# Performance work log

Measured on AMD Instinct MI355X. Metric: run time of the kernel, lower is better.

Reference implementation:

```python
import jax, jax.numpy as jnp
from jax import lax
import numpy as np

B, DIM, H, W = 8, 192, 128, 128
HEADS = 4


def setup_inputs() -> dict:
    key = jax.random.key(0)
    k1, k2, k3, k4 = jax.random.split(key, 4)
    x = jax.random.normal(k1, (B, DIM, H, W), dtype=jnp.float32)
    w_qkv = jax.random.normal(k2, (2 * DIM, DIM), dtype=jnp.float32) * 0.05
    w_dw = jax.random.normal(k3, (2 * DIM, 1, 3, 3), dtype=jnp.float32) * 0.1
    w_proj = jax.random.normal(k4, (DIM, DIM), dtype=jnp.float32) * 0.05
    temperature = jnp.ones((HEADS, 1, 1), dtype=jnp.float32)
    return {"x": x, "w_qkv": w_qkv, "w_dw": w_dw, "w_proj": w_proj, "temperature": temperature}


def reference(x, w_qkv, w_dw, w_proj, temperature):
    b, c, h, w = x.shape
    heads = temperature.shape[0]
    head_c = c // heads
    # 1x1 conv: dim -> 2*dim
    qkv = jnp.einsum('oc,bchw->bohw', w_qkv, x)
    # 3x3 depthwise conv over 2*dim channels
    qkv = lax.conv_general_dilated(
        qkv, w_dw, window_strides=(1, 1), padding='SAME',
        feature_group_count=2 * c,
        dimension_numbers=('NCHW', 'OIHW', 'NCHW'))
    q, v = jnp.split(qkv, 2, axis=1)
    # [b, heads, head_c, h*w]
    q = q.reshape(b, heads, head_c, h * w)
    v = v.reshape(b, heads, head_c, h * w)
    # L2-normalize q over spatial dim; k = q
    q = q / jnp.linalg.norm(q, axis=-1, keepdims=True)
    # channel-wise attention: [b, heads, head_c, head_c]
    attn = jnp.einsum('bhcn,bhdn->bhcd', q, q) * temperature[None]
    attn = jax.nn.softmax(attn, axis=-1)
    out = jnp.einsum('bhcd,bhdn->bhcn', attn, v)
    out = out.reshape(b, c, h, w)
    # 1x1 projection
    return jnp.einsum('oc,bchw->bohw', w_proj, out)
```

## Files before the change

kernel.cpp:

```cpp
#include <hip/hip_runtime.h>

#define BB 8
#define CC 192
#define C2 384
#define HH 128
#define WW 128
#define NN 16384
#define NHEADS 4
#define HC 48
#define LTK 196
#define LTK2 98

typedef float f32x2 __attribute__((ext_vector_type(2)));
typedef float f32x4 __attribute__((ext_vector_type(4)));
typedef float f32x16 __attribute__((ext_vector_type(16)));
typedef short s16x4 __attribute__((ext_vector_type(4)));
typedef short s16x8 __attribute__((ext_vector_type(8)));
typedef unsigned short u16;
typedef u16 u16x4 __attribute__((ext_vector_type(4)));
typedef u16 u16x8 __attribute__((ext_vector_type(8)));
typedef unsigned int u32;

__device__ __forceinline__ float bfu2f(u32 u16v) {
  return __uint_as_float(u16v << 16);
}
__device__ __forceinline__ u16 f2bfu(float f) {
  u32 u = __float_as_uint(f);
  return (u16)((u + 0x7fffu + ((u >> 16) & 1u)) >> 16);
}
__device__ __forceinline__ s16x8 ldpair(const u16* p) {
  s16x4 lo = *reinterpret_cast<const s16x4*>(p);
  s16x4 hi = *reinterpret_cast<const s16x4*>(p + 16);
  return __builtin_shufflevector(lo, hi, 0, 1, 2, 3, 4, 5, 6, 7);
}
__device__ __forceinline__ s16x8 ldb64pair(const u32* p) {
  s16x4 lo = *reinterpret_cast<const s16x4*>(p);
  s16x4 hi = *reinterpret_cast<const s16x4*>(p + 2);
  return __builtin_shufflevector(lo, hi, 0, 1, 2, 3, 4, 5, 6, 7);
}

__global__ __launch_bounds__(256) void k0_wcvt(const float* __restrict__ w,
                                               u16* __restrict__ wbf) {
  const int i = (blockIdx.x * 256 + threadIdx.x) * 4;
  f32x4 v = *reinterpret_cast<const f32x4*>(&w[i]);
  u16x4 o;
  o[0] = f2bfu(v[0]); o[1] = f2bfu(v[1]); o[2] = f2bfu(v[2]); o[3] = f2bfu(v[3]);
  *reinterpret_cast<u16x4*>(&wbf[i]) = o;
}

__global__ __launch_bounds__(512, 4) void k1_qkv(
    const float* __restrict__ x, const u16* __restrict__ wbf,
    u16* __restrict__ qkv) {
  const int bx = blockIdx.x;
  const int n0 = (((bx & 7) << 4) + (bx >> 3)) << 7;
  const int b  = blockIdx.y;
  __shared__ u16 Xs[128 * LTK];
  u32* Xsw = reinterpret_cast<u32*>(Xs);
  const int t = threadIdx.x, lane = t & 63;
  const int wid = t >> 6, wo = wid >> 1, wn = wid & 1;
  const int l31 = lane & 31, g2 = lane >> 5;

  {
    const int nq = t & 31, cr = t >> 5;
    const int kpb = cr >> 1;
    const int jh = cr & 1;
    const int prA = 2 * nq + jh;
    const int prB = 64 + 2 * nq + jh;
    const float* xb = x + (size_t)b * CC * NN + n0 + 4 * nq;
    #pragma unroll 6
    for (int i = 0; i < 12; ++i) {
      f32x4 v = *reinterpret_cast<const f32x4*>(xb + (size_t)(cr + 16 * i) * NN);
      u32 A  = (u32)f2bfu(v[0]) | ((u32)f2bfu(v[1]) << 16);
      u32 Bp = (u32)f2bfu(v[2]) | ((u32)f2bfu(v[3]) << 16);
      u32 oA = __shfl_xor(A, 32);
      u32 oB = __shfl_xor(Bp, 32);
      u32 va, vb;
      if (jh) {
        va = (oB & 0xffffu) | (Bp << 16);
        vb = (oB >> 16) | (Bp & 0xffff0000u);
      } else {
        va = (A & 0xffffu) | (oA << 16);
        vb = (A >> 16) | (oA & 0xffff0000u);
      }
      const int col = kpb + 8 * i;
      Xsw[prA * LTK2 + col] = va;
      Xsw[prB * LTK2 + col] = vb;
    }
  }
  __syncthreads();

  const int nb2 = wn * 32;
  const u32* browE = &Xsw[(nb2 + l31) * LTK2 + 4 * g2];
  const u32* browO = &Xsw[(64 + nb2 + l31) * LTK2 + 4 * g2];

  for (int ot = 0; ot < 3; ++ot) {
    const int o0 = ot * 128;
    const u16* wr = wbf + (size_t)(o0 + wo * 32 + l31) * CC + 8 * g2;

    s16x8 afA[6], afB[6];
    #pragma unroll
    for (int s = 0; s < 6; ++s) {
      afA[s] = *reinterpret_cast<const s16x8*>(wr + s * 32);
      afB[s] = *reinterpret_cast<const s16x8*>(wr + s * 32 + 16);
    }

    f32x16 accE, accO;
    #pragma unroll
    for (int e = 0; e < 16; ++e) { accE[e] = 0.f; accO[e] = 0.f; }

    #pragma unroll
    for (int s = 0; s < 6; ++s) {
      s16x8 bfE0 = ldb64pair(browE + 16 * s);
      s16x8 bfE1 = ldb64pair(browE + 16 * s + 8);
      s16x8 bfO0 = ldb64pair(browO + 16 * s);
      s16x8 bfO1 = ldb64pair(browO + 16 * s + 8);
      accE = __builtin_amdgcn_mfma_f32_32x32x16_bf16(afA[s], bfE0, accE, 0, 0, 0);
      accO = __builtin_amdgcn_mfma_f32_32x32x16_bf16(afA[s], bfO0, accO, 0, 0, 0);
      accE = __builtin_amdgcn_mfma_f32_32x32x16_bf16(afB[s], bfE1, accE, 0, 0, 0);
      accO = __builtin_amdgcn_mfma_f32_32x32x16_bf16(afB[s], bfO1, accO, 0, 0, 0);
    }
    #pragma unroll
    for (int r = 0; r < 16; ++r) {
      const int row = (r & 3) + 8 * (r >> 2) + 4 * g2;
      const u32 pk = (u32)f2bfu(accE[r]) | ((u32)f2bfu(accO[r]) << 16);
      *reinterpret_cast<u32*>(
          &qkv[((size_t)b * C2 + o0 + wo * 32 + row) * NN + n0 + wn * 64 + 2 * l31]) = pk;
    }
  }
}

__global__ __launch_bounds__(256) void k2_dw(
    const u16* __restrict__ qkv, const float* __restrict__ wdw,
    u16* __restrict__ out) {
  const int gid = blockIdx.x;
  const int rb = gid & 7;
  const int p = gid >> 3;
  const int b = p / 192, cv = p % 192;
  const int ch = CC + cv;
  const int plane = b * C2 + ch;
  const int t = threadIdx.x;
  const int row = rb * 16 + (t >> 4);
  const int x0 = (t & 15) * 8;
  const u16* pp = qkv + (size_t)plane * NN;
  const float* wv = wdw + ch * 9;
  float o[8];
  #pragma unroll
  for (int j = 0; j < 8; ++j) o[j] = 0.f;
  #pragma unroll
  for (int dy = 0; dy < 3; ++dy) {
    const int yy = row + dy - 1;
    if ((unsigned)yy < (unsigned)HH) {
      const u16* rp = pp + yy * WW;
      u16x8 m = *reinterpret_cast<const u16x8*>(&rp[x0]);
      float px[10];
      px[0] = (x0 > 0) ? bfu2f(rp[x0 - 1]) : 0.f;
      px[9] = (x0 < 120) ? bfu2f(rp[x0 + 8]) : 0.f;
      #pragma unroll
      for (int j = 0; j < 8; ++j) px[j + 1] = bfu2f(m[j]);
      const float w0 = wv[dy * 3 + 0], w1 = wv[dy * 3 + 1], w2 = wv[dy * 3 + 2];
      #pragma unroll
      for (int j = 0; j < 8; ++j)
        o[j] += w0 * px[j] + w1 * px[j + 1] + w2 * px[j + 2];
    }
  }
  u16x8 ov;
  #pragma unroll
  for (int j = 0; j < 8; ++j) ov[j] = f2bfu(o[j]);
  *reinterpret_cast<u16x8*>(&out[(size_t)plane * NN + row * WW + x0]) = ov;
}

__global__ __launch_bounds__(256, 2) void k23_convgram(
    const u16* __restrict__ qkv, const float* __restrict__ wdw,
    float* __restrict__ gpart) {
  const int raw = blockIdx.x;
  const int rp = ((raw & 7) << 3) + (raw >> 3);
  const int h = blockIdx.y, b = blockIdx.z;
  __shared__ u16 inq[48 * 520];
  __shared__ float wsm[432];
  __shared__ u16 qd[48 * 264];
  const int t = threadIdx.x, lane = t & 63, wv = t >> 6;
  const int l15 = lane & 15, g = lane >> 4;
  const u16* qb = qkv + ((size_t)b * C2 + h * HC) * NN;

  for (int idx = t; idx < 432; idx += 256) wsm[idx] = wdw[h * 432 + idx];
  #pragma unroll
  for (int it = 0; it < 12; ++it) {
    const int idx = t + 256 * it;
    const int ch = idx >> 6, rem = idx & 63;
    const int iy = rem >> 4, grp = rem & 15;
    const int gy = 2 * rp - 1 + iy;
    u16x8 v;
    #pragma unroll
    for (int e = 0; e < 8; ++e) v[e] = 0;
    if ((unsigned)gy < (unsigned)HH)
      v = *reinterpret_cast<const u16x8*>(qb + (size_t)ch * NN + gy * WW + grp * 8);
    *reinterpret_cast<u16x8*>(&inq[ch * 520 + iy * 128 + grp * 8]) = v;
  }
  __syncthreads();

  #pragma unroll
  for (int it = 0; it < 6; ++it) {
    const int idx = t + 256 * it;
    const int ch = idx >> 5, grp = idx & 31;
    const int p0 = grp * 8;
    const int orow = p0 >> 7, x0 = p0 & 127;
    float o[8];
    #pragma unroll
    for (int j = 0; j < 8; ++j) o[j] = 0.f;
    #pragma unroll
    for (int dy = 0; dy < 3; ++dy) {
      const u16* rp_ = &inq[ch * 520 + (orow + dy) * 128];
      u16x8 m = *reinterpret_cast<const u16x8*>(&rp_[x0]);
      float px[10];
      px[0] = (x0 > 0) ? bfu2f(rp_[x0 - 1]) : 0.f;
      px[9] = (x0 < 120) ? bfu2f(rp_[x0 + 8]) : 0.f;
      #pragma unroll
      for (int j = 0; j < 8; ++j) px[j + 1] = bfu2f(m[j]);
      const float w0 = wsm[ch * 9 + dy * 3 + 0];
      const float w1 = wsm[ch * 9 + dy * 3 + 1];
      const float w2 = wsm[ch * 9 + dy * 3 + 2];
      #pragma unroll
      for (int j = 0; j < 8; ++j)
        o[j] += w0 * px[j] + w1 * px[j + 1] + w2 * px[j + 2];
    }
    u16x8 ov;
    #pragma unroll
    for (int j = 0; j < 8; ++j) ov[j] = f2bfu(o[j]);
    *reinterpret_cast<u16x8*>(&qd[ch * 264 + p0]) = ov;
  }
  __syncthreads();

  f32x4 acc[3][3];
  #pragma unroll
  for (int i = 0; i < 3; ++i)
    #pragma unroll
    for (int j = 0; j < 3; ++j)
      #pragma unroll
      for (int e = 0; e < 4; ++e) acc[i][j][e] = 0.f;

  #pragma unroll
  for (int s = 0; s < 2; ++s) {
    const int n = wv * 64 + s * 32;
    s16x8 cf[3];
    #pragma unroll
    for (int i = 0; i < 3; ++i)
      cf[i] = ldpair(&qd[(i * 16 + l15) * 264 + n + 4 * g]);
    #pragma unroll
    for (int i = 0; i < 3; ++i)
      #pragma unroll
      for (int j = 0; j < 3; ++j)
        acc[i][j] = __builtin_amdgcn_mfma_f32_16x16x32_bf16(cf[i], cf[j], acc[i][j], 0, 0, 0);
  }

  float* red = reinterpret_cast<float*>(inq);
  #pragma unroll
  for (int i = 0; i < 3; ++i)
    #pragma unroll
    for (int j = 0; j < 3; ++j)
      #pragma unroll
      for (int r = 0; r < 4; ++r)
        red[wv * 2304 + (i * 16 + 4 * g + r) * 48 + j * 16 + l15] = acc[i][j][r];
  __syncthreads();
  float* gp = gpart + (size_t)b * 3145728 + h * 147456 + rp * 2304;
  for (int idx = t; idx < 2304; idx += 256)
    gp[idx] = red[idx] + red[2304 + idx] + red[4608 + idx] + red[6912 + idx];
}

__global__ __launch_bounds__(256) void k4_soft(
    const float* __restrict__ gpart, const float* __restrict__ temp,
    float* __restrict__ attn) {
  const int bh = blockIdx.x;
  const int b = bh >> 2, h = bh & 3;
  const int t = threadIdx.x;
  __shared__ float G[2304];
  __shared__ float rn[48];
  const float* gp = gpart + (size_t)b * 3145728 + h * 147456;
  for (int idx = t; idx < 2304; idx += 256) {
    float s = 0.f;
    #pragma unroll 8
    for (int c = 0; c < 64; ++c) s += gp[c * 2304 + idx];
    G[idx] = s;
  }
  __syncthreads();
  if (t < 48) rn[t] = rsqrtf(G[t * 48 + t]);
  __syncthreads();
  if (t < 48) {
    const float tm = temp[h];
    float v[48];
    float mx = -1e30f;
    #pragma unroll
    for (int j = 0; j < 48; ++j) {
      v[j] = G[t * 48 + j] * rn[t] * rn[j] * tm;
      mx = fmaxf(mx, v[j]);
    }
    float s = 0.f;
    #pragma unroll
    for (int j = 0; j < 48; ++j) { v[j] = expf(v[j] - mx); s += v[j]; }
    const float inv = 1.f / s;
    #pragma unroll
    for (int j = 0; j < 48; ++j)
      attn[(size_t)bh * 2304 + t * 48 + j] = v[j] * inv;
  }
}

__global__ __launch_bounds__(192) void k5_M(
    const float* __restrict__ wproj, const float* __restrict__ attn,
    u16* __restrict__ Mbf) {
  const int o = blockIdx.x;
  const int b = blockIdx.y;
  const int d = threadIdx.x;
  const int h = d / HC, dl = d % HC;
  const float* wrow = wproj + o * CC + h * HC;
  const float* at = attn + ((size_t)(b * NHEADS + h)) * 2304;
  float s = 0.f;
  #pragma unroll
  for (int c = 0; c < HC; ++c) s = fmaf(wrow[c], at[c * HC + dl], s);
  Mbf[((size_t)b * CC + o) * CC + d] = f2bfu(s);
}

__global__ __launch_bounds__(256, 4) void k6_out(
    const u16* __restrict__ Mbf, const u16* __restrict__ qkvd,
    float* __restrict__ out) {
  const int bx = blockIdx.x;
  const int n0 = (((bx & 7) << 4) + (bx >> 3)) << 7;
  const int b  = blockIdx.y;
  __shared__ u16 Vs[128 * LTK];
  u32* Vsw = reinterpret_cast<u32*>(Vs);
  const int t = threadIdx.x, lane = t & 63;
  const int wid = t >> 6, wo = wid >> 1, wn = wid & 1;
  const int l31 = lane & 31, g2 = lane >> 5;

  {
    const int nq = t & 31, cr = t >> 5;
    const int kpb = cr >> 1;
    const int jh = cr & 1;
    const int prA = 2 * nq + jh;
    const int prB = 64 + 2 * nq + jh;
    const u16* vbp = qkvd + ((size_t)b * C2 + CC) * NN + n0 + 4 * nq;
    #pragma unroll 6
    for (int i = 0; i < 24; ++i) {
      u16x4 m = *reinterpret_cast<const u16x4*>(vbp + (size_t)(cr + 8 * i) * NN);
      u32 A  = (u32)m[0] | ((u32)m[1] << 16);
      u32 Bp = (u32)m[2] | ((u32)m[3] << 16);
      u32 oA = __shfl_xor(A, 32);
      u32 oB = __shfl_xor(Bp, 32);
      u32 va, vb;
      if (jh) {
        va = (oB & 0xffffu) | (Bp << 16);
        vb = (oB >> 16) | (Bp & 0xffff0000u);
      } else {
        va = (A & 0xffffu) | (oA << 16);
        vb = (A >> 16) | (oA & 0xffff0000u);
      }
      const int col = kpb + 4 * i;
      Vsw[prA * LTK2 + col] = va;
      Vsw[prB * LTK2 + col] = vb;
    }
  }
  __syncthreads();

  const int nb2 = wn * 32;
  const u32* browE = &Vsw[(nb2 + l31) * LTK2 + 4 * g2];
  const u32* browO = &Vsw[(64 + nb2 + l31) * LTK2 + 4 * g2];
  const u16* Ab = Mbf + (size_t)b * CC * CC;

  for (int ot = 0; ot < 3; ++ot) {
    const int o0 = ot * 64;
    const u16* ar = Ab + (size_t)(o0 + wo * 32 + l31) * CC + 8 * g2;

    s16x8 afA[6], afB[6];
    #pragma unroll
    for (int s = 0; s < 6; ++s) {
      afA[s] = *reinterpret_cast<const s16x8*>(ar + s * 32);
      afB[s] = *reinterpret_cast<const s16x8*>(ar + s * 32 + 16);
    }

    f32x16 accE, accO;
    #pragma unroll
    for (int e = 0; e < 16; ++e) { accE[e] = 0.f; accO[e] = 0.f; }

    #pragma unroll
    for (int s = 0; s < 6; ++s) {
      s16x8 bfE0 = ldb64pair(browE + 16 * s);
      s16x8 bfE1 = ldb64pair(browE + 16 * s + 8);
      s16x8 bfO0 = ldb64pair(browO + 16 * s);
      s16x8 bfO1 = ldb64pair(browO + 16 * s + 8);
      accE = __builtin_amdgcn_mfma_f32_32x32x16_bf16(afA[s], bfE0, accE, 0, 0, 0);
      accO = __builtin_amdgcn_mfma_f32_32x32x16_bf16(afA[s], bfO0, accO, 0, 0, 0);
      accE = __builtin_amdgcn_mfma_f32_32x32x16_bf16(afB[s], bfE1, accE, 0, 0, 0);
      accO = __builtin_amdgcn_mfma_f32_32x32x16_bf16(afB[s], bfO1, accO, 0, 0, 0);
    }
    #pragma unroll
    for (int r = 0; r < 16; ++r) {
      const int row = (r & 3) + 8 * (r >> 2) + 4 * g2;
      f32x2 st;
      st[0] = accE[r];
      st[1] = accO[r];
      f32x2* op = reinterpret_cast<f32x2*>(
          &out[((size_t)b * CC + o0 + wo * 32 + row) * NN + n0 + wn * 64 + 2 * l31]);
      __builtin_nontemporal_store(st, op);
    }
  }
}

extern "C" void kernel_launch(void* const* d_in, const int* in_sizes, int n_in,
                              void* d_out, int out_size, void* d_ws, size_t ws_size,
                              hipStream_t stream) {
  const float* x      = (const float*)d_in[0];
  const float* w_qkv  = (const float*)d_in[1];
  const float* w_dw   = (const float*)d_in[2];
  const float* w_proj = (const float*)d_in[3];
  const float* temp   = (const float*)d_in[4];
  float* out = (float*)d_out;

  const size_t OFF_QKV   = 0;
  const size_t OFF_QKVD  = 100663296ULL;
  const size_t OFF_ATTN  = 206045184ULL;
  const size_t OFF_M     = 206340096ULL;
  const size_t OFF_WBF   = 206929920ULL;
  const size_t NEEDED    = 207077376ULL;
  if (ws_size < NEEDED) return;

  char* ws = (char*)d_ws;
  u16* qkv   = (u16*)(ws + OFF_QKV);
  u16* qkvd  = (u16*)(ws + OFF_QKVD);
  float* gpart = (float*)(ws + OFF_QKVD);
  float* attn  = (float*)(ws + OFF_ATTN);
  u16* Mbf   = (u16*)(ws + OFF_M);
  u16* wbf   = (u16*)(ws + OFF_WBF);

  k0_wcvt<<<dim3(72), 256, 0, stream>>>(w_qkv, wbf);
  k1_qkv <<<dim3(128, 8), 512, 0, stream>>>(x, wbf, qkv);
  k2_dw  <<<dim3(BB * 192 * 8), 256, 0, stream>>>(qkv, w_dw, qkvd);
  k23_convgram<<<dim3(64, NHEADS, BB), 256, 0, stream>>>(qkv, w_dw, gpart);
  k4_soft<<<dim3(BB * NHEADS), 256, 0, stream>>>(gpart, temp, attn);
  k5_M   <<<dim3(CC, BB), 192, 0, stream>>>(w_proj, attn, Mbf);
  k6_out <<<dim3(128, 8), 256, 0, stream>>>(Mbf, qkvd, out);
}
```

Before: 223.6 us.

## Store qkv and dw-conv output in row-blocked layout for contiguous per-row access

Changes the intermediate qkv and depthwise-conv buffers from channel-plane NCHW to a [b][row][channel][128] blocked layout. k1 writes each 128-pixel row tile for all channels into one contiguous block, and k2 is reorganised to process one image row across all v channels. k23 and k6 read the new layout so their strided loads become contiguous chunks. The gpart region moves to its own offset with a smaller per-batch stride. This is meant to improve DRAM locality of writes and reads across the pipeline, at the cost of k2 doing more work per block and k23 halo loads touching separate blocks.

```diff
diff --git a/kernel.cpp b/kernel.cpp
--- a/kernel.cpp
+++ b/kernel.cpp
@@ -50,9 +50,10 @@
 
 __global__ __launch_bounds__(512, 4) void k1_qkv(
     const float* __restrict__ x, const u16* __restrict__ wbf,
-    u16* __restrict__ qkv) {
+    u16* __restrict__ qblk) {
   const int bx = blockIdx.x;
-  const int n0 = (((bx & 7) << 4) + (bx >> 3)) << 7;
+  const int p0 = ((bx & 7) << 4) + (bx >> 3);
+  const int n0 = p0 << 7;
   const int b  = blockIdx.y;
   __shared__ u16 Xs[128 * LTK];
   u32* Xsw = reinterpret_cast<u32*>(Xs);
@@ -92,6 +93,7 @@
   const int nb2 = wn * 32;
   const u32* browE = &Xsw[(nb2 + l31) * LTK2 + 4 * g2];
   const u32* browO = &Xsw[(64 + nb2 + l31) * LTK2 + 4 * g2];
+  u16* dstbase = qblk + ((size_t)(b * 128 + p0) * C2) * 128;
 
   for (int ot = 0; ot < 3; ++ot) {
     const int o0 = ot * 128;
@@ -124,53 +126,54 @@
       const int row = (r & 3) + 8 * (r >> 2) + 4 * g2;
       const u32 pk = (u32)f2bfu(accE[r]) | ((u32)f2bfu(accO[r]) << 16);
       *reinterpret_cast<u32*>(
-          &qkv[((size_t)b * C2 + o0 + wo * 32 + row) * NN + n0 + wn * 64 + 2 * l31]) = pk;
+          &dstbase[(o0 + wo * 32 + row) * 128 + wn * 64 + 2 * l31]) = pk;
     }
   }
 }
 
 __global__ __launch_bounds__(256) void k2_dw(
-    const u16* __restrict__ qkv, const float* __restrict__ wdw,
-    u16* __restrict__ out) {
-  const int gid = blockIdx.x;
-  const int rb = gid & 7;
-  const int p = gid >> 3;
-  const int b = p / 192, cv = p % 192;
-  const int ch = CC + cv;
-  const int plane = b * C2 + ch;
+    const u16* __restrict__ qblk, const float* __restrict__ wdw,
+    u16* __restrict__ vblk) {
+  const int y = blockIdx.x;
+  const int b = blockIdx.y;
   const int t = threadIdx.x;
-  const int row = rb * 16 + (t >> 4);
-  const int x0 = (t & 15) * 8;
-  const u16* pp = qkv + (size_t)plane * NN;
-  const float* wv = wdw + ch * 9;
-  float o[8];
-  #pragma unroll
-  for (int j = 0; j < 8; ++j) o[j] = 0.f;
-  #pragma unroll
-  for (int dy = 0; dy < 3; ++dy) {
-    const int yy = row + dy - 1;
-    if ((unsigned)yy < (unsigned)HH) {
-      const u16* rp = pp + yy * WW;
-      u16x8 m = *reinterpret_cast<const u16x8*>(&rp[x0]);
-      float px[10];
-      px[0] = (x0 > 0) ? bfu2f(rp[x0 - 1]) : 0.f;
-      px[9] = (x0 < 120) ? bfu2f(rp[x0 + 8]) : 0.f;
-      #pragma unroll
-      for (int j = 0; j < 8; ++j) px[j + 1] = bfu2f(m[j]);
-      const float w0 = wv[dy * 3 + 0], w1 = wv[dy * 3 + 1], w2 = wv[dy * 3 + 2];
-      #pragma unroll
-      for (int j = 0; j < 8; ++j)
-        o[j] += w0 * px[j] + w1 * px[j + 1] + w2 * px[j + 2];
-    }
-  }
-  u16x8 ov;
-  #pragma unroll
-  for (int j = 0; j < 8; ++j) ov[j] = f2bfu(o[j]);
-  *reinterpret_cast<u16x8*>(&out[(size_t)plane * NN + row * WW + x0]) = ov;
+  #pragma unroll
+  for (int it = 0; it < 12; ++it) {
+    const int idx = t + 256 * it;
+    const int ch = idx >> 4;
+    const int grp = idx & 15;
+    const int x0 = grp * 8;
+    const float* wv = wdw + (CC + ch) * 9;
+    float o[8];
+    #pragma unroll
+    for (int j = 0; j < 8; ++j) o[j] = 0.f;
+    #pragma unroll
+    for (int dy = 0; dy < 3; ++dy) {
+      const int gy = y + dy - 1;
+      if ((unsigned)gy < (unsigned)HH) {
+        const u16* rp = qblk + ((size_t)(b * 128 + gy) * C2 + CC + ch) * 128;
+        u16x8 m = *reinterpret_cast<const u16x8*>(&rp[x0]);
+        float px[10];
+        px[0] = (x0 > 0) ? bfu2f(rp[x0 - 1]) : 0.f;
+        px[9] = (x0 < 120) ? bfu2f(rp[x0 + 8]) : 0.f;
+        #pragma unroll
+        for (int j = 0; j < 8; ++j) px[j + 1] = bfu2f(m[j]);
+        const float w0 = wv[dy * 3 + 0], w1 = wv[dy * 3 + 1], w2 = wv[dy * 3 + 2];
+        #pragma unroll
+        for (int j = 0; j < 8; ++j)
+          o[j] += w0 * px[j] + w1 * px[j + 1] + w2 * px[j + 2];
+      }
+    }
+    u16x8 ov;
+    #pragma unroll
+    for (int j = 0; j < 8; ++j) ov[j] = f2bfu(o[j]);
+    *reinterpret_cast<u16x8*>(
+        &vblk[((size_t)(b * 128 + y) * 192 + ch) * 128 + x0]) = ov;
+  }
 }
 
 __global__ __launch_bounds__(256, 2) void k23_convgram(
-    const u16* __restrict__ qkv, const float* __restrict__ wdw,
+    const u16* __restrict__ qblk, const float* __restrict__ wdw,
     float* __restrict__ gpart) {
   const int raw = blockIdx.x;
   const int rp = ((raw & 7) << 3) + (raw >> 3);
@@ -180,7 +183,6 @@
   __shared__ u16 qd[48 * 264];
   const int t = threadIdx.x, lane = t & 63, wv = t >> 6;
   const int l15 = lane & 15, g = lane >> 4;
-  const u16* qb = qkv + ((size_t)b * C2 + h * HC) * NN;
 
   for (int idx = t; idx < 432; idx += 256) wsm[idx] = wdw[h * 432 + idx];
   #pragma unroll
@@ -193,7 +195,8 @@
     #pragma unroll
     for (int e = 0; e < 8; ++e) v[e] = 0;
     if ((unsigned)gy < (unsigned)HH)
-      v = *reinterpret_cast<const u16x8*>(qb + (size_t)ch * NN + gy * WW + grp * 8);
+      v = *reinterpret_cast<const u16x8*>(
+          qblk + ((size_t)(b * 128 + gy) * C2 + h * HC + ch) * 128 + grp * 8);
     *reinterpret_cast<u16x8*>(&inq[ch * 520 + iy * 128 + grp * 8]) = v;
   }
   __syncthreads();
@@ -261,7 +264,7 @@
       for (int r = 0; r < 4; ++r)
         red[wv * 2304 + (i * 16 + 4 * g + r) * 48 + j * 16 + l15] = acc[i][j][r];
   __syncthreads();
-  float* gp = gpart + (size_t)b * 3145728 + h * 147456 + rp * 2304;
+  float* gp = gpart + (size_t)b * 589824 + h * 147456 + rp * 2304;
   for (int idx = t; idx < 2304; idx += 256)
     gp[idx] = red[idx] + red[2304 + idx] + red[4608 + idx] + red[6912 + idx];
 }
@@ -274,7 +277,7 @@
   const int t = threadIdx.x;
   __shared__ float G[2304];
   __shared__ float rn[48];
-  const float* gp = gpart + (size_t)b * 3145728 + h * 147456;
+  const float* gp = gpart + (size_t)b * 589824 + h * 147456;
   for (int idx = t; idx < 2304; idx += 256) {
     float s = 0.f;
     #pragma unroll 8
@@ -319,10 +322,11 @@
 }
 
 __global__ __launch_bounds__(256, 4) void k6_out(
-    const u16* __restrict__ Mbf, const u16* __restrict__ qkvd,
+    const u16* __restrict__ Mbf, const u16* __restrict__ vblk,
     float* __restrict__ out) {
   const int bx = blockIdx.x;
-  const int n0 = (((bx & 7) << 4) + (bx >> 3)) << 7;
+  const int p0 = ((bx & 7) << 4) + (bx >> 3);
+  const int n0 = p0 << 7;
   const int b  = blockIdx.y;
   __shared__ u16 Vs[128 * LTK];
   u32* Vsw = reinterpret_cast<u32*>(Vs);
@@ -336,10 +340,10 @@
     const int jh = cr & 1;
     const int prA = 2 * nq + jh;
     const int prB = 64 + 2 * nq + jh;
-    const u16* vbp = qkvd + ((size_t)b * C2 + CC) * NN + n0 + 4 * nq;
+    const u16* vbp = vblk + (size_t)(b * 128 + p0) * 192 * 128 + 4 * nq;
     #pragma unroll 6
     for (int i = 0; i < 24; ++i) {
-      u16x4 m = *reinterpret_cast<const u16x4*>(vbp + (size_t)(cr + 8 * i) * NN);
+      u16x4 m = *reinterpret_cast<const u16x4*>(vbp + (cr + 8 * i) * 128);
       u32 A  = (u32)m[0] | ((u32)m[1] << 16);
       u32 Bp = (u32)m[2] | ((u32)m[3] << 16);
       u32 oA = __shfl_xor(A, 32);
@@ -414,7 +418,8 @@
   float* out = (float*)d_out;
 
   const size_t OFF_QKV   = 0;
-  const size_t OFF_QKVD  = 100663296ULL;
+  const size_t OFF_VDW   = 100663296ULL;
+  const size_t OFF_GPART = 150994944ULL;
   const size_t OFF_ATTN  = 206045184ULL;
   const size_t OFF_M     = 206340096ULL;
   const size_t OFF_WBF   = 206929920ULL;
@@ -422,18 +427,18 @@
   if (ws_size < NEEDED) return;
 
   char* ws = (char*)d_ws;
-  u16* qkv   = (u16*)(ws + OFF_QKV);
-  u16* qkvd  = (u16*)(ws + OFF_QKVD);
-  float* gpart = (float*)(ws + OFF_QKVD);
+  u16* qblk  = (u16*)(ws + OFF_QKV);
+  u16* vblk  = (u16*)(ws + OFF_VDW);
+  float* gpart = (float*)(ws + OFF_GPART);
   float* attn  = (float*)(ws + OFF_ATTN);
   u16* Mbf   = (u16*)(ws + OFF_M);
   u16* wbf   = (u16*)(ws + OFF_WBF);
 
   k0_wcvt<<<dim3(72), 256, 0, stream>>>(w_qkv, wbf);
-  k1_qkv <<<dim3(128, 8), 512, 0, stream>>>(x, wbf, qkv);
-  k2_dw  <<<dim3(BB * 192 * 8), 256, 0, stream>>>(qkv, w_dw, qkvd);
-  k23_convgram<<<dim3(64, NHEADS, BB), 256, 0, stream>>>(qkv, w_dw, gpart);
+  k1_qkv <<<dim3(128, 8), 512, 0, stream>>>(x, wbf, qblk);
+  k2_dw  <<<dim3(128, 8), 256, 0, stream>>>(qblk, w_dw, vblk);
+  k23_convgram<<<dim3(64, NHEADS, BB), 256, 0, stream>>>(qblk, w_dw, gpart);
   k4_soft<<<dim3(BB * NHEADS), 256, 0, stream>>>(gpart, temp, attn);
   k5_M   <<<dim3(CC, BB), 192, 0, stream>>>(w_proj, attn, Mbf);
-  k6_out <<<dim3(128, 8), 256, 0, stream>>>(Mbf, qkvd, out);
-}
+  k6_out <<<dim3(128, 8), 256, 0, stream>>>(Mbf, vblk, out);
+}
```

Result: slower. 253.9 us (+13.6%).
